# Kernel optimization log

Hardware: AMD Instinct MI355X
Metric: run time of the kernel (lower is better)

## Reference

```python
import jax, jax.numpy as jnp
import numpy as np
from math import sqrt

B, NQ, SK, ISIZE, HSIZE, OSIZE, H = 4, 2048, 2048, 1024, 1024, 1024, 16
D = HSIZE // H  # attn_dim = 64
IEPS = 1e-32
NEG = -1e32

def setup_inputs() -> dict:
    key = jax.random.key(0)
    ks = jax.random.split(key, 9)
    scale = 1.0 / sqrt(ISIZE)
    return {
        "iQ": jax.random.normal(ks[0], (B, NQ, ISIZE), jnp.float32),
        "iK": jax.random.normal(ks[1], (B, SK, ISIZE), jnp.float32),
        "iV": jax.random.normal(ks[2], (B, SK, ISIZE), jnp.float32),
        "mask": jax.random.randint(ks[3], (B, NQ, SK), 0, 2).astype(bool),
        # torch nn.Linear weights: [out_features, in_features]
        "Wq": jax.random.normal(ks[4], (HSIZE, ISIZE), jnp.float32) * scale,
        "Wk": jax.random.normal(ks[5], (HSIZE, ISIZE), jnp.float32) * scale,
        "Wv": jax.random.normal(ks[6], (HSIZE, ISIZE), jnp.float32) * scale,
        "Wo": jax.random.normal(ks[7], (OSIZE, HSIZE), jnp.float32) * scale,
        "sn_bias": jnp.zeros((1,), jnp.float32),  # SparseNormer bias
    }

def reference(iQ, iK, iV, mask, Wq, Wk, Wv, Wo, sn_bias):
    b, nq, _ = iQ.shape
    sk = iK.shape[1]
    # projections, split into heads: [b, h, n, d]
    q = (iQ @ Wq.T).reshape(b, nq, H, D).transpose(0, 2, 1, 3)
    k = (iK @ Wk.T).reshape(b, sk, H, D).transpose(0, 2, 1, 3)
    v = (iV @ Wv.T).reshape(b, sk, H, D).transpose(0, 2, 1, 3)
    # scaled dot-product scores: [b, h, nq, sk]
    scores = jnp.einsum("bhqd,bhkd->bhqk", q, k) / sqrt(D)
    scores = jnp.where(mask[:, None, :, :], NEG, scores)
    # SparseNormer: relu(x + bias)^2 normalized along last dim
    t = jax.nn.relu(scores + sn_bias)
    t = t * t
    attn = t / (t.sum(-1, keepdims=True) + IEPS)
    o = jnp.einsum("bhqk,bhkd->bhqd", attn, v)
    o = o.transpose(0, 2, 1, 3).reshape(b, nq, HSIZE)
    return o @ Wo.T
```

## Files before the change

kernel.cpp:

```cpp
#include <hip/hip_runtime.h>
#include <stdint.h>

#define B_   4
#define NQ_  2048
#define SK_  2048
#define H_   16
#define HS_  1024
#define D_   64

typedef __attribute__((ext_vector_type(8))) short bf16x8;
typedef __attribute__((ext_vector_type(4))) float f32x4;
typedef __attribute__((ext_vector_type(8))) unsigned short u16x8;
typedef __attribute__((ext_vector_type(4))) int i32x4;

#define DEVI __device__ __forceinline__

DEVI unsigned short f2bf_hu(float f) {
  union { float f; unsigned int i; } x; x.f = f;
  return (unsigned short)((x.i + 0x8000u) >> 16);
}
DEVI unsigned int pack2(float a, float b) {
  union { float f; unsigned int i; } x, y; x.f = a; y.f = b;
  return __builtin_amdgcn_perm(y.i + 0x8000u, x.i + 0x8000u, 0x07060302u);
}
DEVI u16x8 cvt8(f32x4 lo, f32x4 hi) {
  union { u16x8 s; unsigned int w[4]; } r;
  r.w[0] = pack2(lo[0], lo[1]);
  r.w[1] = pack2(lo[2], lo[3]);
  r.w[2] = pack2(hi[0], hi[1]);
  r.w[3] = pack2(hi[2], hi[3]);
  return r.s;
}
DEVI void async16(void* lds, const void* g) {
  __builtin_amdgcn_global_load_lds(
      (const __attribute__((address_space(1))) unsigned int*)g,
      (__attribute__((address_space(3))) unsigned int*)lds, 16, 0, 0);
}

__global__ __launch_bounds__(256)
void cvt_prep(const float* __restrict__ a, unsigned short* __restrict__ ab,
              const float* __restrict__ wsrc, unsigned short* __restrict__ wdst,
              int naBlocks) {
  const int bi = blockIdx.x;
  const float* s; unsigned short* d; size_t base;
  if (bi < naBlocks) { s = a;    d = ab;   base = (size_t)bi * 2048; }
  else               { s = wsrc; d = wdst; base = (size_t)(bi - naBlocks) * 2048; }
  const size_t o = base + (size_t)threadIdx.x * 8;
  f32x4 lo = *(const f32x4*)(s + o);
  f32x4 hi = *(const f32x4*)(s + o + 4);
  *(u16x8*)(d + o) = cvt8(lo, hi);
}

__global__ __launch_bounds__(256)
void pack_mask(const int* __restrict__ m, unsigned long long* __restrict__ bits) {
  const size_t tid = (size_t)blockIdx.x * 256 + threadIdx.x;
  const unsigned long long bal = __ballot(m[tid] != 0);
  if ((threadIdx.x & 63) == 0) bits[tid >> 6] = bal;
}

template <bool CF32>
__global__ __launch_bounds__(256)
void gemm_bb(const unsigned short* __restrict__ A, const unsigned short* __restrict__ Wb,
             void* __restrict__ Cp, int M, int N, int K) {
  __shared__ unsigned short As[128 * 32];
  __shared__ unsigned short Bs[128 * 32];
  const int t = threadIdx.x;
  const int w = t >> 6, l = t & 63;
  const int lm = l & 15, lg = l >> 4;
  const int bm = blockIdx.x * 128, bn = blockIdx.y * 128;
  const int wm = (w >> 1) * 64, wn = (w & 1) * 64;

  const int sr = t >> 2;
  const int sg = ((t & 3) ^ ((t >> 3) & 3)) * 8;
  const unsigned short* Ag0 = A + (size_t)(bm + sr) * K + sg;
  const unsigned short* Ag1 = A + (size_t)(bm + sr + 64) * K + sg;
  const unsigned short* Wg0 = Wb + (size_t)(bn + sr) * K + sg;
  const unsigned short* Wg1 = Wb + (size_t)(bn + sr + 64) * K + sg;
  unsigned short* lA0 = &As[t * 8];
  unsigned short* lA1 = &As[t * 8 + 2048];
  unsigned short* lB0 = &Bs[t * 8];
  unsigned short* lB1 = &Bs[t * 8 + 2048];

  const int fx = (lm >> 1) & 3;
  f32x4 acc[4][4] = {};

  for (int k0 = 0; k0 < K; k0 += 32) {
    async16(lA0, Ag0 + k0);
    async16(lA1, Ag1 + k0);
    async16(lB0, Wg0 + k0);
    async16(lB1, Wg1 + k0);
    __syncthreads();
    bf16x8 aF[4], bF[4];
#pragma unroll
    for (int i = 0; i < 4; i++)
      aF[i] = *(const bf16x8*)&As[(wm + i * 16 + lm) * 32 + ((lg ^ fx) * 8)];
#pragma unroll
    for (int i = 0; i < 4; i++)
      bF[i] = *(const bf16x8*)&Bs[(wn + i * 16 + lm) * 32 + ((lg ^ fx) * 8)];
#pragma unroll
    for (int i = 0; i < 4; i++)
#pragma unroll
      for (int j = 0; j < 4; j++)
        acc[i][j] = __builtin_amdgcn_mfma_f32_16x16x32_bf16(aF[i], bF[j], acc[i][j], 0, 0, 0);
    __syncthreads();
  }
#pragma unroll
  for (int i = 0; i < 4; i++)
#pragma unroll
    for (int j = 0; j < 4; j++) {
      const int row = bm + wm + i * 16 + lg * 4;
      const int col = bn + wn + j * 16 + lm;
#pragma unroll
      for (int r = 0; r < 4; r++) {
        if constexpr (CF32) {
          ((float*)Cp)[(size_t)(row + r) * N + col] = acc[i][j][r];
        } else {
          ((unsigned short*)Cp)[(size_t)(row + r) * N + col] = f2bf_hu(acc[i][j][r]);
        }
      }
    }
}

template <bool ABF16, bool CF32>
__global__ __launch_bounds__(256)
void gemm_bt(const void* __restrict__ Ap, const float* __restrict__ W,
             void* __restrict__ Cp, int M, int N, int K) {
  __shared__ unsigned short As[128 * 40];
  __shared__ unsigned short Bs[128 * 40];
  const int t = threadIdx.x;
  const int w = t >> 6, l = t & 63;
  const int lm = l & 15, lg = l >> 4;
  const int bm = blockIdx.x * 128, bn = blockIdx.y * 128;
  const int wm = (w >> 1) * 64, wn = (w & 1) * 64;
  const int sr = t >> 2, sc = (t & 3) * 8;
  const float* Af = (const float*)Ap;
  const unsigned short* Ab = (const unsigned short*)Ap;
  const size_t ao0 = (size_t)(bm + sr) * K + sc;
  const size_t ao1 = (size_t)(bm + sr + 64) * K + sc;
  const size_t wo0 = (size_t)(bn + sr) * K + sc;
  const size_t wo1 = (size_t)(bn + sr + 64) * K + sc;
  auto loadA = [&](size_t off) -> u16x8 {
    if constexpr (ABF16) {
      return *(const u16x8*)(Ab + off);
    } else {
      f32x4 lo = *(const f32x4*)(Af + off);
      f32x4 hi = *(const f32x4*)(Af + off + 4);
      return cvt8(lo, hi);
    }
  };
  auto loadW = [&](size_t off) -> u16x8 {
    f32x4 lo = *(const f32x4*)(W + off);
    f32x4 hi = *(const f32x4*)(W + off + 4);
    return cvt8(lo, hi);
  };
  u16x8 pa0 = loadA(ao0), pa1 = loadA(ao1);
  u16x8 pb0 = loadW(wo0), pb1 = loadW(wo1);
  f32x4 acc[4][4] = {};
  for (int k0 = 0; k0 < K; k0 += 32) {
    *(u16x8*)&As[sr * 40 + sc]        = pa0;
    *(u16x8*)&As[(sr + 64) * 40 + sc] = pa1;
    *(u16x8*)&Bs[sr * 40 + sc]        = pb0;
    *(u16x8*)&Bs[(sr + 64) * 40 + sc] = pb1;
    __syncthreads();
    if (k0 + 32 < K) {
      pa0 = loadA(ao0 + k0 + 32);
      pa1 = loadA(ao1 + k0 + 32);
      pb0 = loadW(wo0 + k0 + 32);
      pb1 = loadW(wo1 + k0 + 32);
    }
    bf16x8 aF[4], bF[4];
#pragma unroll
    for (int i = 0; i < 4; i++)
      aF[i] = *(const bf16x8*)&As[(wm + i * 16 + lm) * 40 + lg * 8];
#pragma unroll
    for (int i = 0; i < 4; i++)
      bF[i] = *(const bf16x8*)&Bs[(wn + i * 16 + lm) * 40 + lg * 8];
#pragma unroll
    for (int i = 0; i < 4; i++)
#pragma unroll
      for (int j = 0; j < 4; j++)
        acc[i][j] = __builtin_amdgcn_mfma_f32_16x16x32_bf16(aF[i], bF[j], acc[i][j], 0, 0, 0);
    __syncthreads();
  }
#pragma unroll
  for (int i = 0; i < 4; i++)
#pragma unroll
    for (int j = 0; j < 4; j++) {
      const int row = bm + wm + i * 16 + lg * 4;
      const int col = bn + wn + j * 16 + lm;
#pragma unroll
      for (int r = 0; r < 4; r++) {
        if constexpr (CF32) {
          ((float*)Cp)[(size_t)(row + r) * N + col] = acc[i][j][r];
        } else {
          ((unsigned short*)Cp)[(size_t)(row + r) * N + col] = f2bf_hu(acc[i][j][r]);
        }
      }
    }
}

template <bool BITMASK>
__global__ __launch_bounds__(256)
void attn_sn(const unsigned short* __restrict__ Qb,
             const unsigned short* __restrict__ Kb,
             const unsigned short* __restrict__ Vb,
             const int* __restrict__ mask,
             const unsigned int* __restrict__ bits,
             const float* __restrict__ snb,
             unsigned short* __restrict__ Ob) {
  __shared__ unsigned short Ks[64 * 72];
  __shared__ unsigned short Vt[64 * 72];
  __shared__ unsigned short Pq[128 * 72];
  __shared__ float denomS[128];

  const int h = blockIdx.x, qt = blockIdx.y, b = blockIdx.z;
  const int t = threadIdx.x, w = t >> 6, l = t & 63;
  const int lm = l & 15, lg = l >> 4;
  const int q0 = qt * 128;
  const int wk = (w >> 1) * 32;
  const int wn = (w & 1) * 64;
  const float bias = snb[0];

  bf16x8 bQ[4][2];
#pragma unroll
  for (int ni = 0; ni < 4; ni++)
#pragma unroll
    for (int kf = 0; kf < 2; kf++) {
      const int qq = q0 + wn + ni * 16 + lm;
      bQ[ni][kf] = *(const bf16x8*)&Qb[(size_t)(b * NQ_ + qq) * HS_ + h * D_ + kf * 32 + lg * 8];
    }

  const int kr = t >> 3, kc = (t & 7) * 8;
  const unsigned short* Kg = Kb + (size_t)(b * SK_) * HS_ + h * D_ + kc;
  const int va = t & 31;
  const int vc = (t >> 5) * 8;
  const unsigned short* Vg = Vb + (size_t)(b * SK_) * HS_ + h * D_ + vc;
  const int* mbase = mask + (size_t)b * NQ_ * SK_;

  f32x4 oacc[2][4] = {};
  float dpart[4] = {0.f, 0.f, 0.f, 0.f};

  u16x8 pk0 = *(const u16x8*)(Kg + (size_t)(kr) * HS_);
  u16x8 pk1 = *(const u16x8*)(Kg + (size_t)(32 + kr) * HS_);
  u16x8 pv0 = *(const u16x8*)(Vg + (size_t)(2 * va) * HS_);
  u16x8 pv1 = *(const u16x8*)(Vg + (size_t)(2 * va + 1) * HS_);

  for (int kt = 0; kt < SK_ / 64; kt++) {
    const int kk0 = kt * 64;
    *(u16x8*)&Ks[kr * 72 + kc]        = pk0;
    *(u16x8*)&Ks[(kr + 32) * 72 + kc] = pk1;
    {
      union { u16x8 s; unsigned int w4[4]; } a0, a1;
      a0.s = pv0; a1.s = pv1;
#pragma unroll
      for (int ww = 0; ww < 4; ww++) {
        unsigned int lo = __builtin_amdgcn_perm(a1.w4[ww], a0.w4[ww], 0x05040100u);
        unsigned int hi = __builtin_amdgcn_perm(a1.w4[ww], a0.w4[ww], 0x07060302u);
        *(unsigned int*)&Vt[(vc + 2 * ww) * 72 + 2 * va]     = lo;
        *(unsigned int*)&Vt[(vc + 2 * ww + 1) * 72 + 2 * va] = hi;
      }
    }
    __syncthreads();

    if (kt + 1 < SK_ / 64) {
      const int nk0 = kk0 + 64;
      pk0 = *(const u16x8*)(Kg + (size_t)(nk0 + kr) * HS_);
      pk1 = *(const u16x8*)(Kg + (size_t)(nk0 + 32 + kr) * HS_);
      pv0 = *(const u16x8*)(Vg + (size_t)(nk0 + 2 * va) * HS_);
      pv1 = *(const u16x8*)(Vg + (size_t)(nk0 + 2 * va + 1) * HS_);
    }
    i32x4 mq[4][2];
    unsigned int mb[4];
    if constexpr (BITMASK) {
#pragma unroll
      for (int ni = 0; ni < 4; ni++)
        mb[ni] = bits[(size_t)(b * NQ_ + q0 + wn + ni * 16 + lm) * 64 + kt * 2 + (wk >> 5)];
    } else {
#pragma unroll
      for (int ni = 0; ni < 4; ni++) {
        const int* mrow = mbase + (size_t)(q0 + wn + ni * 16 + lm) * SK_ + kk0 + wk + lg * 4;
#pragma unroll
        for (int mi = 0; mi < 2; mi++) mq[ni][mi] = *(const i32x4*)(mrow + mi * 16);
      }
    }

    bf16x8 aK[2][2];
#pragma unroll
    for (int mi = 0; mi < 2; mi++)
#pragma unroll
      for (int kf = 0; kf < 2; kf++)
        aK[mi][kf] = *(const bf16x8*)&Ks[(wk + mi * 16 + lm) * 72 + kf * 32 + lg * 8];
    f32x4 sf[2][4] = {};
#pragma unroll
    for (int mi = 0; mi < 2; mi++)
#pragma unroll
      for (int ni = 0; ni < 4; ni++) {
        sf[mi][ni] = __builtin_amdgcn_mfma_f32_16x16x32_bf16(aK[mi][0], bQ[ni][0], sf[mi][ni], 0, 0, 0);
        sf[mi][ni] = __builtin_amdgcn_mfma_f32_16x16x32_bf16(aK[mi][1], bQ[ni][1], sf[mi][ni], 0, 0, 0);
      }

#pragma unroll
    for (int ni = 0; ni < 4; ni++) {
      float dsum = 0.f;
#pragma unroll
      for (int mi = 0; mi < 2; mi++) {
        const f32x4 sv = sf[mi][ni];
        float x2[4];
#pragma unroll
        for (int r = 0; r < 4; r++) {
          float x = fmaxf(sv[r] * 0.125f + bias, 0.f);
          if constexpr (BITMASK) {
            x = ((mb[ni] >> (mi * 16 + lg * 4 + r)) & 1u) ? 0.f : x;
          } else {
            x = mq[ni][mi][r] ? 0.f : x;
          }
          x2[r] = x * x;
          dsum += x2[r];
        }
        const unsigned long long pk =
            (unsigned long long)pack2(x2[0], x2[1]) |
            ((unsigned long long)pack2(x2[2], x2[3]) << 32);
        *(unsigned long long*)&Pq[(wn + ni * 16 + lm) * 72 + wk + mi * 16 + lg * 4] = pk;
      }
      dpart[ni] += dsum;
    }
    __syncthreads();

#pragma unroll
    for (int k2 = 0; k2 < 2; k2++) {
      bf16x8 aV[2], bP[4];
#pragma unroll
      for (int mi = 0; mi < 2; mi++)
        aV[mi] = *(const bf16x8*)&Vt[(wk + mi * 16 + lm) * 72 + k2 * 32 + lg * 8];
#pragma unroll
      for (int ni = 0; ni < 4; ni++)
        bP[ni] = *(const bf16x8*)&Pq[(wn + ni * 16 + lm) * 72 + k2 * 32 + lg * 8];
#pragma unroll
      for (int mi = 0; mi < 2; mi++)
#pragma unroll
        for (int ni = 0; ni < 4; ni++)
          oacc[mi][ni] = __builtin_amdgcn_mfma_f32_16x16x32_bf16(aV[mi], bP[ni], oacc[mi][ni], 0, 0, 0);
    }
    __syncthreads();
  }

#pragma unroll
  for (int ni = 0; ni < 4; ni++) {
    float v = dpart[ni];
    v += __shfl_xor(v, 16, 64);
    v += __shfl_xor(v, 32, 64);
    dpart[ni] = v;
  }
  if (((w >> 1) == 0) && (lg == 0)) {
#pragma unroll
    for (int ni = 0; ni < 4; ni++) denomS[wn + ni * 16 + lm] = dpart[ni];
  }
  __syncthreads();
  if (((w >> 1) == 1) && (lg == 0)) {
#pragma unroll
    for (int ni = 0; ni < 4; ni++) denomS[wn + ni * 16 + lm] += dpart[ni];
  }
  __syncthreads();

#pragma unroll
  for (int ni = 0; ni < 4; ni++) {
    const int ql = wn + ni * 16 + lm;
    const float inv = 1.0f / (denomS[ql] + 1e-32f);
#pragma unroll
    for (int mi = 0; mi < 2; mi++) {
      const int d0 = wk + mi * 16 + lg * 4;
      const f32x4 ov = oacc[mi][ni];
      const unsigned long long pk =
          (unsigned long long)pack2(ov[0] * inv, ov[1] * inv) |
          ((unsigned long long)pack2(ov[2] * inv, ov[3] * inv) << 32);
      *(unsigned long long*)&Pq[ql * 72 + d0] = pk;
    }
  }
  __syncthreads();
  const int qf = t >> 1;
  const int dg = (t & 1) * 32;
  unsigned short* orow = Ob + (size_t)(b * NQ_ + q0 + qf) * HS_ + h * D_ + dg;
#pragma unroll
  for (int j = 0; j < 4; j++) {
    u16x8 vv = *(const u16x8*)&Pq[qf * 72 + dg + j * 8];
    *(u16x8*)(orow + j * 8) = vv;
  }
}

extern "C" void kernel_launch(void* const* d_in, const int* in_sizes, int n_in,
                              void* d_out, int out_size, void* d_ws, size_t ws_size,
                              hipStream_t stream) {
  (void)in_sizes; (void)n_in; (void)out_size;
  const float* iQ  = (const float*)d_in[0];
  const float* iK  = (const float*)d_in[1];
  const float* iV  = (const float*)d_in[2];
  const int*   msk = (const int*)d_in[3];
  const float* Wq  = (const float*)d_in[4];
  const float* Wk  = (const float*)d_in[5];
  const float* Wv  = (const float*)d_in[6];
  const float* Wo  = (const float*)d_in[7];
  const float* snb = (const float*)d_in[8];
  float* out = (float*)d_out;

  const size_t TOK = (size_t)B_ * NQ_ * HS_;
  const size_t WE  = (size_t)HS_ * HS_;
  const size_t BITS_B = (size_t)B_ * NQ_ * SK_ / 8;
  const size_t NEED = (3 * TOK + WE) * 2 + BITS_B;

  const dim3 gg(64, 8, 1), bb(256, 1, 1);
  const dim3 ga(H_, NQ_ / 128, B_);
  const int M = B_ * NQ_, N = HS_, K = HS_;

  if (ws_size >= NEED) {
    unsigned short* Kb = (unsigned short*)d_ws;
    unsigned short* Vb = Kb + TOK;
    unsigned short* Ob = Vb + TOK;
    unsigned short* Wb = Ob + TOK;
    unsigned int* bits = (unsigned int*)(Wb + WE);
    unsigned short* out_us = (unsigned short*)d_out;
    unsigned short* Qb  = out_us;
    unsigned short* INb = out_us + TOK;

    hipLaunchKernelGGL(cvt_prep, dim3(4608), bb, 0, stream, iQ, INb, Wq, Wb, 4096);
    hipLaunchKernelGGL((gemm_bb<false>), gg, bb, 0, stream, INb, Wb, (void*)Qb, M, N, K);
    hipLaunchKernelGGL(cvt_prep, dim3(4608), bb, 0, stream, iK, INb, Wk, Wb, 4096);
    hipLaunchKernelGGL((gemm_bb<false>), gg, bb, 0, stream, INb, Wb, (void*)Kb, M, N, K);
    hipLaunchKernelGGL(cvt_prep, dim3(4608), bb, 0, stream, iV, INb, Wv, Wb, 4096);
    hipLaunchKernelGGL((gemm_bb<false>), gg, bb, 0, stream, INb, Wb, (void*)Vb, M, N, K);
    hipLaunchKernelGGL(cvt_prep, dim3(512), bb, 0, stream,
                       (const float*)nullptr, (unsigned short*)nullptr, Wo, Wb, 0);
    hipLaunchKernelGGL(pack_mask, dim3(65536), bb, 0, stream,
                       msk, (unsigned long long*)bits);
    hipLaunchKernelGGL((attn_sn<true>), ga, bb, 0, stream,
                       Qb, Kb, Vb, msk, bits, snb, Ob);
    hipLaunchKernelGGL((gemm_bb<true>), gg, bb, 0, stream, Ob, Wb, (void*)out, M, N, K);
  } else {
    unsigned short *Qb, *Kb, *Vb, *Ob;
    if (ws_size >= 4 * TOK * sizeof(unsigned short)) {
      Qb = (unsigned short*)d_ws;
      Kb = Qb + TOK;
      Vb = Qb + 2 * TOK;
      Ob = Qb + 3 * TOK;
    } else {
      Qb = (unsigned short*)d_out;
      Kb = (unsigned short*)d_ws;
      Vb = Kb + TOK;
      Ob = Kb + 2 * TOK;
    }
    hipLaunchKernelGGL((gemm_bt<false, false>), gg, bb, 0, stream, (const void*)iQ, Wq, (void*)Qb, M, N, K);
    hipLaunchKernelGGL((gemm_bt<false, false>), gg, bb, 0, stream, (const void*)iK, Wk, (void*)Kb, M, N, K);
    hipLaunchKernelGGL((gemm_bt<false, false>), gg, bb, 0, stream, (const void*)iV, Wv, (void*)Vb, M, N, K);
    hipLaunchKernelGGL((attn_sn<false>), ga, bb, 0, stream,
                       Qb, Kb, Vb, msk, (const unsigned int*)nullptr, snb, Ob);
    hipLaunchKernelGGL((gemm_bt<true, true>), gg, bb, 0, stream, (const void*)Ob, Wo, (void*)out, M, N, K);
  }
}
```

Before: 485.2 us.

## Use precomputed float additive mask, XOR-swizzled LDS, packed FP32 math in attention

Adds a mask_madd pre-pass that turns the boolean mask into a float additive tensor (bias or -1e9). When the workspace is large enough, the attention kernel reads that tensor and applies mask, scale and bias with packed FMA/mul/add. LDS tiles drop the 72-wide padding in favour of an XOR swizzle, MFMA sections are wrapped in setprio, and launch bounds request 4 blocks per CU. The cost is that the attention kernel now reads a 4-byte-per-element mask (128 MB of fp32) instead of a bit-packed one, a large increase in memory traffic.

```diff
diff --git a/kernel.cpp b/kernel.cpp
--- a/kernel.cpp
+++ b/kernel.cpp
@@ -10,6 +10,7 @@
 
 typedef __attribute__((ext_vector_type(8))) short bf16x8;
 typedef __attribute__((ext_vector_type(4))) float f32x4;
+typedef __attribute__((ext_vector_type(2))) float f32x2;
 typedef __attribute__((ext_vector_type(8))) unsigned short u16x8;
 typedef __attribute__((ext_vector_type(4))) int i32x4;
 
@@ -36,6 +37,29 @@
       (const __attribute__((address_space(1))) unsigned int*)g,
       (__attribute__((address_space(3))) unsigned int*)lds, 16, 0, 0);
 }
+
+DEVI f32x2 pkfma(f32x2 a, f32x2 b, f32x2 c) {
+  f32x2 d;
+  asm("v_pk_fma_f32 %0, %1, %2, %3" : "=v"(d) : "v"(a), "v"(b), "v"(c));
+  return d;
+}
+DEVI f32x2 pkmul(f32x2 a, f32x2 b) {
+  f32x2 d;
+  asm("v_pk_mul_f32 %0, %1, %2" : "=v"(d) : "v"(a), "v"(b));
+  return d;
+}
+DEVI f32x2 pkadd(f32x2 a, f32x2 b) {
+  f32x2 d;
+  asm("v_pk_add_f32 %0, %1, %2" : "=v"(d) : "v"(a), "v"(b));
+  return d;
+}
+DEVI unsigned int cvtpk_bf16(float lo, float hi) {
+  unsigned int r;
+  asm("v_cvt_pk_bf16_f32 %0, %1, %2" : "=v"(r) : "v"(lo), "v"(hi));
+  return r;
+}
+
+#define SWZB(row, colb) ((((row) * 128) + (colb)) ^ (((row) & 7) << 4))
 
 __global__ __launch_bounds__(256)
 void cvt_prep(const float* __restrict__ a, unsigned short* __restrict__ ab,
@@ -56,6 +80,18 @@
   const size_t tid = (size_t)blockIdx.x * 256 + threadIdx.x;
   const unsigned long long bal = __ballot(m[tid] != 0);
   if ((threadIdx.x & 63) == 0) bits[tid >> 6] = bal;
+}
+
+__global__ __launch_bounds__(256)
+void mask_madd(const int* __restrict__ m, float* __restrict__ madd,
+               const float* __restrict__ snb) {
+  const float bias = snb[0];
+  const size_t i = ((size_t)blockIdx.x * 256 + threadIdx.x) * 4;
+  const i32x4 mv = *(const i32x4*)(m + i);
+  f32x4 o;
+#pragma unroll
+  for (int r = 0; r < 4; r++) o[r] = mv[r] ? -1e9f : bias;
+  *(f32x4*)(madd + i) = o;
 }
 
 template <bool CF32>
@@ -199,19 +235,19 @@
     }
 }
 
-template <bool BITMASK>
-__global__ __launch_bounds__(256)
+template <int MODE>
+__global__ __launch_bounds__(256, 4)
 void attn_sn(const unsigned short* __restrict__ Qb,
              const unsigned short* __restrict__ Kb,
              const unsigned short* __restrict__ Vb,
              const int* __restrict__ mask,
              const unsigned int* __restrict__ bits,
+             const float* __restrict__ madd,
              const float* __restrict__ snb,
              unsigned short* __restrict__ Ob) {
-  __shared__ unsigned short Ks[64 * 72];
-  __shared__ unsigned short Vt[64 * 72];
-  __shared__ unsigned short Pq[128 * 72];
-  __shared__ float denomS[128];
+  __shared__ unsigned short Ks[64 * 64];
+  __shared__ unsigned short Vt[64 * 64];
+  __shared__ unsigned short Pq[128 * 64];
 
   const int h = blockIdx.x, qt = blockIdx.y, b = blockIdx.z;
   const int t = threadIdx.x, w = t >> 6, l = t & 63;
@@ -221,6 +257,10 @@
   const int wn = (w & 1) * 64;
   const float bias = snb[0];
 
+  char* KsB = (char*)Ks;
+  char* VtB = (char*)Vt;
+  char* PqB = (char*)Pq;
+
   bf16x8 bQ[4][2];
 #pragma unroll
   for (int ni = 0; ni < 4; ni++)
@@ -230,15 +270,22 @@
       bQ[ni][kf] = *(const bf16x8*)&Qb[(size_t)(b * NQ_ + qq) * HS_ + h * D_ + kf * 32 + lg * 8];
     }
 
-  const int kr = t >> 3, kc = (t & 7) * 8;
-  const unsigned short* Kg = Kb + (size_t)(b * SK_) * HS_ + h * D_ + kc;
+  const int kr = t >> 3, kcb = (t & 7) * 16;
+  const unsigned short* Kg = Kb + (size_t)(b * SK_) * HS_ + h * D_ + (t & 7) * 8;
   const int va = t & 31;
   const int vc = (t >> 5) * 8;
   const unsigned short* Vg = Vb + (size_t)(b * SK_) * HS_ + h * D_ + vc;
   const int* mbase = mask + (size_t)b * NQ_ * SK_;
+  const float* Mg[4];
+  if constexpr (MODE == 2) {
+#pragma unroll
+    for (int ni = 0; ni < 4; ni++)
+      Mg[ni] = madd + (size_t)(b * NQ_ + q0 + wn + ni * 16 + lm) * SK_ + wk + lg * 4;
+  }
 
   f32x4 oacc[2][4] = {};
   float dpart[4] = {0.f, 0.f, 0.f, 0.f};
+  f32x2 dp2[4] = {};
 
   u16x8 pk0 = *(const u16x8*)(Kg + (size_t)(kr) * HS_);
   u16x8 pk1 = *(const u16x8*)(Kg + (size_t)(32 + kr) * HS_);
@@ -247,8 +294,8 @@
 
   for (int kt = 0; kt < SK_ / 64; kt++) {
     const int kk0 = kt * 64;
-    *(u16x8*)&Ks[kr * 72 + kc]        = pk0;
-    *(u16x8*)&Ks[(kr + 32) * 72 + kc] = pk1;
+    *(u16x8*)(KsB + SWZB(kr, kcb))      = pk0;
+    *(u16x8*)(KsB + SWZB(kr + 32, kcb)) = pk1;
     {
       union { u16x8 s; unsigned int w4[4]; } a0, a1;
       a0.s = pv0; a1.s = pv1;
@@ -256,8 +303,8 @@
       for (int ww = 0; ww < 4; ww++) {
         unsigned int lo = __builtin_amdgcn_perm(a1.w4[ww], a0.w4[ww], 0x05040100u);
         unsigned int hi = __builtin_amdgcn_perm(a1.w4[ww], a0.w4[ww], 0x07060302u);
-        *(unsigned int*)&Vt[(vc + 2 * ww) * 72 + 2 * va]     = lo;
-        *(unsigned int*)&Vt[(vc + 2 * ww + 1) * 72 + 2 * va] = hi;
+        *(unsigned int*)(VtB + SWZB(vc + 2 * ww,     4 * va)) = lo;
+        *(unsigned int*)(VtB + SWZB(vc + 2 * ww + 1, 4 * va)) = hi;
       }
     }
     __syncthreads();
@@ -269,9 +316,17 @@
       pv0 = *(const u16x8*)(Vg + (size_t)(nk0 + 2 * va) * HS_);
       pv1 = *(const u16x8*)(Vg + (size_t)(nk0 + 2 * va + 1) * HS_);
     }
+
+    f32x4 ma[4][2];
     i32x4 mq[4][2];
     unsigned int mb[4];
-    if constexpr (BITMASK) {
+    if constexpr (MODE == 2) {
+#pragma unroll
+      for (int ni = 0; ni < 4; ni++)
+#pragma unroll
+        for (int mi = 0; mi < 2; mi++)
+          ma[ni][mi] = *(const f32x4*)(Mg[ni] + kk0 + mi * 16);
+    } else if constexpr (MODE == 1) {
 #pragma unroll
       for (int ni = 0; ni < 4; ni++)
         mb[ni] = bits[(size_t)(b * NQ_ + q0 + wn + ni * 16 + lm) * 64 + kt * 2 + (wk >> 5)];
@@ -289,8 +344,9 @@
     for (int mi = 0; mi < 2; mi++)
 #pragma unroll
       for (int kf = 0; kf < 2; kf++)
-        aK[mi][kf] = *(const bf16x8*)&Ks[(wk + mi * 16 + lm) * 72 + kf * 32 + lg * 8];
+        aK[mi][kf] = *(const bf16x8*)(KsB + SWZB(wk + mi * 16 + lm, kf * 64 + lg * 16));
     f32x4 sf[2][4] = {};
+    __builtin_amdgcn_s_setprio(1);
 #pragma unroll
     for (int mi = 0; mi < 2; mi++)
 #pragma unroll
@@ -298,31 +354,56 @@
         sf[mi][ni] = __builtin_amdgcn_mfma_f32_16x16x32_bf16(aK[mi][0], bQ[ni][0], sf[mi][ni], 0, 0, 0);
         sf[mi][ni] = __builtin_amdgcn_mfma_f32_16x16x32_bf16(aK[mi][1], bQ[ni][1], sf[mi][ni], 0, 0, 0);
       }
-
-#pragma unroll
-    for (int ni = 0; ni < 4; ni++) {
-      float dsum = 0.f;
-#pragma unroll
-      for (int mi = 0; mi < 2; mi++) {
-        const f32x4 sv = sf[mi][ni];
-        float x2[4];
-#pragma unroll
-        for (int r = 0; r < 4; r++) {
-          float x = fmaxf(sv[r] * 0.125f + bias, 0.f);
-          if constexpr (BITMASK) {
-            x = ((mb[ni] >> (mi * 16 + lg * 4 + r)) & 1u) ? 0.f : x;
-          } else {
-            x = mq[ni][mi][r] ? 0.f : x;
+    __builtin_amdgcn_s_setprio(0);
+
+    if constexpr (MODE == 2) {
+      const f32x2 c8 = {0.125f, 0.125f};
+#pragma unroll
+      for (int ni = 0; ni < 4; ni++) {
+#pragma unroll
+        for (int mi = 0; mi < 2; mi++) {
+          const f32x4 sv = sf[mi][ni];
+          const f32x4 mv = ma[ni][mi];
+          f32x2 t01 = pkfma((f32x2){sv[0], sv[1]}, c8, (f32x2){mv[0], mv[1]});
+          f32x2 t23 = pkfma((f32x2){sv[2], sv[3]}, c8, (f32x2){mv[2], mv[3]});
+          t01[0] = fmaxf(t01[0], 0.f); t01[1] = fmaxf(t01[1], 0.f);
+          t23[0] = fmaxf(t23[0], 0.f); t23[1] = fmaxf(t23[1], 0.f);
+          const f32x2 u01 = pkmul(t01, t01);
+          const f32x2 u23 = pkmul(t23, t23);
+          dp2[ni] = pkadd(dp2[ni], u01);
+          dp2[ni] = pkadd(dp2[ni], u23);
+          const unsigned long long pk =
+              (unsigned long long)cvtpk_bf16(u01[0], u01[1]) |
+              ((unsigned long long)cvtpk_bf16(u23[0], u23[1]) << 32);
+          *(unsigned long long*)(PqB + SWZB(wn + ni * 16 + lm, (wk + mi * 16 + lg * 4) * 2)) = pk;
+        }
+      }
+    } else {
+#pragma unroll
+      for (int ni = 0; ni < 4; ni++) {
+        float dsum = 0.f;
+#pragma unroll
+        for (int mi = 0; mi < 2; mi++) {
+          const f32x4 sv = sf[mi][ni];
+          float x2[4];
+#pragma unroll
+          for (int r = 0; r < 4; r++) {
+            float x = fmaxf(sv[r] * 0.125f + bias, 0.f);
+            if constexpr (MODE == 1) {
+              x = ((mb[ni] >> (mi * 16 + lg * 4 + r)) & 1u) ? 0.f : x;
+            } else {
+              x = mq[ni][mi][r] ? 0.f : x;
+            }
+            x2[r] = x * x;
+            dsum += x2[r];
           }
-          x2[r] = x * x;
-          dsum += x2[r];
+          const unsigned long long pk =
+              (unsigned long long)pack2(x2[0], x2[1]) |
+              ((unsigned long long)pack2(x2[2], x2[3]) << 32);
+          *(unsigned long long*)(PqB + SWZB(wn + ni * 16 + lm, (wk + mi * 16 + lg * 4) * 2)) = pk;
         }
-        const unsigned long long pk =
-            (unsigned long long)pack2(x2[0], x2[1]) |
-            ((unsigned long long)pack2(x2[2], x2[3]) << 32);
-        *(unsigned long long*)&Pq[(wn + ni * 16 + lm) * 72 + wk + mi * 16 + lg * 4] = pk;
-      }
-      dpart[ni] += dsum;
+        dpart[ni] += dsum;
+      }
     }
     __syncthreads();
 
@@ -331,22 +412,25 @@
       bf16x8 aV[2], bP[4];
 #pragma unroll
       for (int mi = 0; mi < 2; mi++)
-        aV[mi] = *(const bf16x8*)&Vt[(wk + mi * 16 + lm) * 72 + k2 * 32 + lg * 8];
+        aV[mi] = *(const bf16x8*)(VtB + SWZB(wk + mi * 16 + lm, k2 * 64 + lg * 16));
 #pragma unroll
       for (int ni = 0; ni < 4; ni++)
-        bP[ni] = *(const bf16x8*)&Pq[(wn + ni * 16 + lm) * 72 + k2 * 32 + lg * 8];
+        bP[ni] = *(const bf16x8*)(PqB + SWZB(wn + ni * 16 + lm, k2 * 64 + lg * 16));
+      __builtin_amdgcn_s_setprio(1);
 #pragma unroll
       for (int mi = 0; mi < 2; mi++)
 #pragma unroll
         for (int ni = 0; ni < 4; ni++)
           oacc[mi][ni] = __builtin_amdgcn_mfma_f32_16x16x32_bf16(aV[mi], bP[ni], oacc[mi][ni], 0, 0, 0);
-    }
-    __syncthreads();
-  }
-
+      __builtin_amdgcn_s_setprio(0);
+    }
+    __syncthreads();
+  }
+
+  float* denomS = (float*)Ks;
 #pragma unroll
   for (int ni = 0; ni < 4; ni++) {
-    float v = dpart[ni];
+    float v = (MODE == 2) ? (dp2[ni][0] + dp2[ni][1]) : dpart[ni];
     v += __shfl_xor(v, 16, 64);
     v += __shfl_xor(v, 32, 64);
     dpart[ni] = v;
@@ -371,18 +455,17 @@
       const int d0 = wk + mi * 16 + lg * 4;
       const f32x4 ov = oacc[mi][ni];
       const unsigned long long pk =
-          (unsigned long long)pack2(ov[0] * inv, ov[1] * inv) |
-          ((unsigned long long)pack2(ov[2] * inv, ov[3] * inv) << 32);
-      *(unsigned long long*)&Pq[ql * 72 + d0] = pk;
+          (unsigned long long)cvtpk_bf16(ov[0] * inv, ov[1] * inv) |
+          ((unsigned long long)cvtpk_bf16(ov[2] * inv, ov[3] * inv) << 32);
+      *(unsigned long long*)(PqB + SWZB(ql, d0 * 2)) = pk;
     }
   }
   __syncthreads();
   const int qf = t >> 1;
-  const int dg = (t & 1) * 32;
-  unsigned short* orow = Ob + (size_t)(b * NQ_ + q0 + qf) * HS_ + h * D_ + dg;
+  unsigned short* orow = Ob + (size_t)(b * NQ_ + q0 + qf) * HS_ + h * D_ + (t & 1) * 32;
 #pragma unroll
   for (int j = 0; j < 4; j++) {
-    u16x8 vv = *(const u16x8*)&Pq[qf * 72 + dg + j * 8];
+    u16x8 vv = *(const u16x8*)(PqB + SWZB(qf, (t & 1) * 64 + j * 16));
     *(u16x8*)(orow + j * 8) = vv;
   }
 }
@@ -405,21 +488,25 @@
   const size_t TOK = (size_t)B_ * NQ_ * HS_;
   const size_t WE  = (size_t)HS_ * HS_;
   const size_t BITS_B = (size_t)B_ * NQ_ * SK_ / 8;
-  const size_t NEED = (3 * TOK + WE) * 2 + BITS_B;
+  const size_t MADD_B = (size_t)B_ * NQ_ * SK_ * 4;
+  const size_t NEED1 = (3 * TOK + WE) * 2 + BITS_B;
+  const size_t NEED2 = NEED1 + MADD_B;
 
   const dim3 gg(64, 8, 1), bb(256, 1, 1);
   const dim3 ga(H_, NQ_ / 128, B_);
   const int M = B_ * NQ_, N = HS_, K = HS_;
 
-  if (ws_size >= NEED) {
+  if (ws_size >= NEED1) {
     unsigned short* Kb = (unsigned short*)d_ws;
     unsigned short* Vb = Kb + TOK;
     unsigned short* Ob = Vb + TOK;
     unsigned short* Wb = Ob + TOK;
     unsigned int* bits = (unsigned int*)(Wb + WE);
+    float* madd = (float*)((char*)bits + BITS_B);
     unsigned short* out_us = (unsigned short*)d_out;
     unsigned short* Qb  = out_us;
     unsigned short* INb = out_us + TOK;
+    const bool useMadd = (ws_size >= NEED2);
 
     hipLaunchKernelGGL(cvt_prep, dim3(4608), bb, 0, stream, iQ, INb, Wq, Wb, 4096);
     hipLaunchKernelGGL((gemm_bb<false>), gg, bb, 0, stream, INb, Wb, (void*)Qb, M, N, K);
@@ -429,10 +516,16 @@
     hipLaunchKernelGGL((gemm_bb<false>), gg, bb, 0, stream, INb, Wb, (void*)Vb, M, N, K);
     hipLaunchKernelGGL(cvt_prep, dim3(512), bb, 0, stream,
                        (const float*)nullptr, (unsigned short*)nullptr, Wo, Wb, 0);
-    hipLaunchKernelGGL(pack_mask, dim3(65536), bb, 0, stream,
-                       msk, (unsigned long long*)bits);
-    hipLaunchKernelGGL((attn_sn<true>), ga, bb, 0, stream,
-                       Qb, Kb, Vb, msk, bits, snb, Ob);
+    if (useMadd) {
+      hipLaunchKernelGGL(mask_madd, dim3(16384), bb, 0, stream, msk, madd, snb);
+      hipLaunchKernelGGL((attn_sn<2>), ga, bb, 0, stream,
+                         Qb, Kb, Vb, msk, (const unsigned int*)nullptr, madd, snb, Ob);
+    } else {
+      hipLaunchKernelGGL(pack_mask, dim3(65536), bb, 0, stream,
+                         msk, (unsigned long long*)bits);
+      hipLaunchKernelGGL((attn_sn<1>), ga, bb, 0, stream,
+                         Qb, Kb, Vb, msk, bits, (const float*)nullptr, snb, Ob);
+    }
     hipLaunchKernelGGL((gemm_bb<true>), gg, bb, 0, stream, Ob, Wb, (void*)out, M, N, K);
   } else {
     unsigned short *Qb, *Kb, *Vb, *Ob;
@@ -450,8 +543,9 @@
     hipLaunchKernelGGL((gemm_bt<false, false>), gg, bb, 0, stream, (const void*)iQ, Wq, (void*)Qb, M, N, K);
     hipLaunchKernelGGL((gemm_bt<false, false>), gg, bb, 0, stream, (const void*)iK, Wk, (void*)Kb, M, N, K);
     hipLaunchKernelGGL((gemm_bt<false, false>), gg, bb, 0, stream, (const void*)iV, Wv, (void*)Vb, M, N, K);
-    hipLaunchKernelGGL((attn_sn<false>), ga, bb, 0, stream,
-                       Qb, Kb, Vb, msk, (const unsigned int*)nullptr, snb, Ob);
+    hipLaunchKernelGGL((attn_sn<0>), ga, bb, 0, stream,
+                       Qb, Kb, Vb, msk, (const unsigned int*)nullptr,
+                       (const float*)nullptr, snb, Ob);
     hipLaunchKernelGGL((gemm_bt<true, true>), gg, bb, 0, stream, (const void*)Ob, Wo, (void*)out, M, N, K);
   }
 }
```

Result: slower. 1.155 ms (+138.0%).
